# Kernel optimization log

Measured on AMD Instinct MI355X. Metric: run time of the kernel, lower is better.

The kernel has to match this reference:

```python
import jax, jax.numpy as jnp
import numpy as np

B = 256
IN_CH = 1
E = 8          # embedding_channels (power of 2)
DEPTH = 3      # log2(E)
T = 8192       # time_range
WINDOW = 2.0
K = 15         # kernel_size (odd -> torch 'same' == lax 'SAME')
TPI = 2.0 * np.pi


def conv1d(x, w, b, dilation=1, groups=1):
    # x: (B, Cin, T), w: (Cout, Cin/groups, K), b: (Cout,)
    out = jax.lax.conv_general_dilated(
        x, w, window_strides=(1,), padding='SAME',
        rhs_dilation=(dilation,),
        dimension_numbers=('NCH', 'OIH', 'NCH'),
        feature_group_count=groups)
    return out + b[None, :, None]


def setup_inputs() -> dict:
    key = jax.random.key(0)
    ks = jax.random.split(key, 14)
    s = 0.05
    x = jax.random.normal(ks[0], (B, T), jnp.float32)
    W1 = jax.random.normal(ks[1], (E, 2, 1, K), jnp.float32) * s   # per-channel Conv1d(1,2)
    b1 = jax.random.normal(ks[2], (E, 2), jnp.float32) * s
    W2 = jax.random.normal(ks[3], (E, 1, 2, K), jnp.float32) * s   # per-channel Conv1d(2,1)
    b2 = jax.random.normal(ks[4], (E, 1), jnp.float32) * s
    fcW = jax.random.normal(ks[5], (E, 2, T), jnp.float32) * 0.01  # per-channel Linear(T, 2)
    fcb = jax.random.normal(ks[6], (E, 2), jnp.float32) * s
    # deconv tree: level j has 2**(DEPTH-1-j) Conv1d(2,1) units, stacked as grouped conv
    dW0 = jax.random.normal(ks[7], (4, 2, K), jnp.float32) * s
    db0 = jax.random.normal(ks[8], (4,), jnp.float32) * s
    dW1 = jax.random.normal(ks[9], (2, 2, K), jnp.float32) * s
    db1 = jax.random.normal(ks[10], (2,), jnp.float32) * s
    dW2 = jax.random.normal(ks[11], (1, 2, K), jnp.float32) * s
    db2 = jax.random.normal(ks[12], (1,), jnp.float32) * s
    return dict(x=x, W1=W1, b1=b1, W2=W2, b2=b2, fcW=fcW, fcb=fcb,
                dW0=dW0, db0=db0, dW1=dW1, db1=db1, dW2=dW2, db2=db2)


def reference(x, W1, b1, W2, b2, fcW, fcb, dW0, db0, dW1, db1, dW2, db2):
    y = x.reshape(x.shape[0], IN_CH, T)
    # per-channel dilated conv stack (dilation = 2**i)
    chans = []
    for i in range(E):
        h = conv1d(y, W1[i], b1[i], dilation=2 ** i)
        chans.append(conv1d(h, W2[i], b2[i], dilation=2 ** i))
    latent = jnp.concatenate(chans, axis=1)                # (B, E, T)
    # FFT -> frequency / amplitude / offset
    rfft = jnp.fft.rfft(latent, axis=2)                    # (B, E, T//2+1)
    power = jnp.abs(rfft[:, :, 1:]) ** 2
    freqs = jnp.asarray(np.fft.rfftfreq(T)[1:] * T / WINDOW, jnp.float32)
    psum = jnp.sum(power, axis=2)
    f = jnp.sum(freqs * power, axis=2) / psum              # (B, E)
    a = 2.0 * jnp.sqrt(psum) / T
    b_off = rfft.real[:, :, 0] / T
    # per-channel Linear(T, 2) -> phase
    v = jnp.einsum('bet,ect->bec', latent, fcW) + fcb      # (B, E, 2)
    p = jnp.arctan2(v[..., 1], v[..., 0]) / TPI            # (B, E)
    # sinusoid reconstruction
    args = jnp.linspace(-WINDOW / 2, WINDOW / 2, T, dtype=jnp.float32)
    sig = a[..., None] * jnp.sin(TPI * (f[..., None] * args + p[..., None])) + b_off[..., None]
    # deconv tree: pairs of channels -> grouped conv, halving channels each level
    y = sig
    for dW, db in ((dW0, db0), (dW1, db1), (dW2, db2)):
        y = conv1d(y, dW, db, dilation=1, groups=dW.shape[0])
    out = y.reshape(y.shape[0], IN_CH * T)
    return (out, latent, sig,
            p[..., None], f[..., None], a[..., None], b_off[..., None])
```

## Files before the change

kernel.cpp:

```cpp
#include <hip/hip_runtime.h>
#include <math.h>

#define TT 8192
#define BB 256
#define EE 8
#define KK 15
#define PI_F  3.14159265358979323846f
#define TPI_F 6.28318530717958647692f

#define OFF_OUT 0
#define OFF_LAT (BB*TT)
#define OFF_SIG (OFF_LAT + BB*EE*TT)
#define OFF_P   (OFF_SIG + BB*EE*TT)
#define OFF_F   (OFF_P + BB*EE)
#define OFF_A   (OFF_F + BB*EE)
#define OFF_B0  (OFF_A + BB*EE)

#define SWZ(i) ((i) + ((i) >> 5))
#define NF 4096

#define L_RE   0
#define L_IM   4223
#define L_SW   8446
#define L_RBUF 8542
#define L_TOT  8574

__device__ __forceinline__ float rdfl(float v) {
  return __uint_as_float(__builtin_amdgcn_readfirstlane(__float_as_uint(v)));
}

__device__ __forceinline__ int rev4(int k) {
  unsigned r = __brev((unsigned)k) >> 20;
  return (int)(((r & 0x555u) << 1) | ((r >> 1) & 0x555u));
}

__global__ __launch_bounds__(512) void conv_fft_kernel(
    const float* __restrict__ x, const float* __restrict__ W1,
    const float* __restrict__ b1, const float* __restrict__ W2,
    const float* __restrict__ b2, const float* __restrict__ fcW,
    const float* __restrict__ fcb, float* __restrict__ latent,
    float* __restrict__ outP, float* __restrict__ outF,
    float* __restrict__ outA, float* __restrict__ outB0)
{
  extern __shared__ float smem[];
  float* re   = smem + L_RE;
  float* im   = smem + L_IM;
  float* sW   = smem + L_SW;
  float* rbuf = smem + L_RBUF;

  const int e = blockIdx.x, b = blockIdx.y;
  const int d  = 1 << e;
  const int M  = TT >> e;
  const int tid = threadIdx.x;
  const float* xr = x + b * TT;

  if (tid < 29) {
    float acc = 0.0f;
    for (int c = 0; c < 2; c++) {
      const float* w1 = W1 + e*30 + c*15;
      const float* w2 = W2 + e*30 + c*15;
      int jlo = tid - 14; if (jlo < 0) jlo = 0;
      int jhi = tid;      if (jhi > 14) jhi = 14;
      for (int j = jlo; j <= jhi; j++) acc += w2[j] * w1[tid - j];
    }
    sW[tid] = acc;
  } else if (tid == 29) {
    float s20 = 0.f, s21 = 0.f;
    for (int j = 0; j < 15; j++) { s20 += W2[e*30 + j]; s21 += W2[e*30 + 15 + j]; }
    sW[29] = b2[e] + s20*b1[e*2] + s21*b1[e*2 + 1];
  } else if (tid >= 32 && tid < 62) {
    sW[tid] = W1[e*30 + (tid - 32)];
  } else if (tid >= 64 && tid < 94) {
    sW[tid] = W2[e*30 + (tid - 64)];
  } else if (tid == 94 || tid == 95) {
    sW[tid] = b1[e*2 + (tid - 94)];
  }
  __syncthreads();

  float Wc[29];
  #pragma unroll
  for (int s = 0; s < 29; s++) Wc[s] = rdfl(sW[s]);
  const float Bc = rdfl(sW[29]);

  float* lr = latent + (b * EE + e) * TT;

  #pragma unroll 1
  for (int g = 0; g < 4; g++) {
    const int vt = g * 512 + tid;
    const int ph = vt & (d - 1);
    const int m0 = (vt >> e) << 2;
    const float* xp = xr + ph;
    const int nbase = m0 - 14;

    float win[32];
    if (m0 >= 16 && m0 <= M - 20) {
      #pragma unroll
      for (int s = 0; s < 32; s++) win[s] = xp[(nbase + s) * d];
    } else {
      #pragma unroll
      for (int s = 0; s < 32; s++) {
        int ns = nbase + s;
        win[s] = ((unsigned)ns < (unsigned)M) ? xp[ns * d] : 0.0f;
      }
    }

    float acc[4] = {Bc, Bc, Bc, Bc};
    #pragma unroll
    for (int s = 0; s < 29; s++) {
      #pragma unroll
      for (int r = 0; r < 4; r++) acc[r] = fmaf(Wc[s], win[s + r], acc[r]);
    }

    if (m0 <= 6) {
      #pragma unroll
      for (int r = 0; r < 4; r++) {
        float corr = 0.0f;
        #pragma unroll
        for (int j = 0; j < 7; j++) {
          if (m0 + r + j <= 6) {
            float a0 = sW[94], a1 = sW[95];
            #pragma unroll
            for (int k = 0; k < 15; k++) {
              float xv = win[r + j + k];
              a0 = fmaf(sW[32 + k], xv, a0);
              a1 = fmaf(sW[47 + k], xv, a1);
            }
            corr = fmaf(sW[64 + j], a0, corr);
            corr = fmaf(sW[79 + j], a1, corr);
          }
        }
        acc[r] -= corr;
      }
    }
    if (m0 + 3 >= M - 7) {
      #pragma unroll
      for (int r = 0; r < 4; r++) {
        float corr = 0.0f;
        #pragma unroll
        for (int jj = 0; jj < 7; jj++) {
          const int j = 8 + jj;
          if (m0 + r + j >= M + 7) {
            float a0 = sW[94], a1 = sW[95];
            #pragma unroll
            for (int k = 0; k < 15; k++) {
              float xv = win[r + j + k];
              a0 = fmaf(sW[32 + k], xv, a0);
              a1 = fmaf(sW[47 + k], xv, a1);
            }
            corr = fmaf(sW[64 + j], a0, corr);
            corr = fmaf(sW[79 + j], a1, corr);
          }
        }
        acc[r] -= corr;
      }
    }

    #pragma unroll
    for (int r = 0; r < 4; r++) {
      int tg = ph + (m0 + r) * d;
      lr[tg] = acc[r];
      int n  = tg >> 1;
      float* dst = (tg & 1) ? im : re;
      dst[SWZ(n)] = acc[r];
    }
  }
  __syncthreads();

  const float2* f02 = (const float2*)(fcW + (e*2 + 0)*TT);
  const float2* f12 = (const float2*)(fcW + (e*2 + 1)*TT);
  float v0 = 0.f, v1 = 0.f;
  for (int n = tid; n < NF; n += 512) {
    float zr = re[SWZ(n)], zi = im[SWZ(n)];
    float2 a0 = f02[n], a1 = f12[n];
    v0 = fmaf(zr, a0.x, v0); v0 = fmaf(zi, a0.y, v0);
    v1 = fmaf(zr, a1.x, v1); v1 = fmaf(zi, a1.y, v1);
  }
  __syncthreads();

  for (int L = NF >> 2; L >= 1; L >>= 2) {
    float wstep = -1.57079632679f / (float)L;
    for (int u = tid; u < (NF >> 2); u += 512) {
      int p = u & (L - 1);
      int base = ((u - p) << 2) + p;
      int i0 = SWZ(base), i1 = SWZ(base + L), i2 = SWZ(base + 2*L), i3 = SWZ(base + 3*L);
      float ar = re[i0], ai = im[i0];
      float br = re[i1], bi = im[i1];
      float cr = re[i2], ci = im[i2];
      float dr = re[i3], di = im[i3];
      float t0r = ar + cr, t0i = ai + ci;
      float t1r = ar - cr, t1i = ai - ci;
      float t2r = br + dr, t2i = bi + di;
      float t3r = br - dr, t3i = bi - di;
      float A0r = t0r + t2r, A0i = t0i + t2i;
      float A1r = t1r + t3i, A1i = t1i - t3r;
      float A2r = t0r - t2r, A2i = t0i - t2i;
      float A3r = t1r - t3i, A3i = t1i + t3r;
      float ang = wstep * (float)p;
      float s1 = __sinf(ang), c1 = __cosf(ang);
      float c2 = c1*c1 - s1*s1, s2 = 2.f*c1*s1;
      float c3 = c1*c2 - s1*s2, s3 = c1*s2 + s1*c2;
      re[i0] = A0r;                 im[i0] = A0i;
      re[i1] = A1r*c1 - A1i*s1;     im[i1] = A1r*s1 + A1i*c1;
      re[i2] = A2r*c2 - A2i*s2;     im[i2] = A2r*s2 + A2i*c2;
      re[i3] = A3r*c3 - A3i*s3;     im[i3] = A3r*s3 + A3i*c3;
    }
    __syncthreads();
  }

  float pacc = 0.f, facc = 0.f;
  for (int k = 1 + tid; k < NF; k += 512) {
    int jk = SWZ(rev4(k));
    int jm = SWZ(rev4(NF - k));
    float zr = re[jk], zi = im[jk];
    float yr = re[jm], yi = im[jm];
    float Er = 0.5f*(zr + yr), Ei = 0.5f*(zi - yi);
    float Dr = 0.5f*(zr - yr), Di = 0.5f*(zi + yi);
    float Or = Di, Oi = -Dr;
    float ang = -PI_F * (float)k / (float)NF;
    float s = __sinf(ang), c = __cosf(ang);
    float Xr = Er + c*Or - s*Oi;
    float Xi = Ei + c*Oi + s*Or;
    float mag = fmaf(Xr, Xr, Xi*Xi);
    pacc += mag;
    facc = fmaf(0.5f * (float)k, mag, facc);
  }
  if (tid == 0) {
    float X = re[SWZ(0)] - im[SWZ(0)];
    pacc += X*X;
    facc += 2048.0f * X*X;
  }

  #pragma unroll
  for (int off = 32; off > 0; off >>= 1) {
    pacc += __shfl_down(pacc, off);
    facc += __shfl_down(facc, off);
    v0   += __shfl_down(v0, off);
    v1   += __shfl_down(v1, off);
  }
  int wid = tid >> 6, lane = tid & 63;
  if (lane == 0) {
    rbuf[wid*4 + 0] = pacc; rbuf[wid*4 + 1] = facc;
    rbuf[wid*4 + 2] = v0;   rbuf[wid*4 + 3] = v1;
  }
  __syncthreads();
  if (tid == 0) {
    float P = 0.f, Fw = 0.f, V0 = 0.f, V1 = 0.f;
    #pragma unroll
    for (int w = 0; w < 8; w++) {
      P += rbuf[w*4]; Fw += rbuf[w*4+1]; V0 += rbuf[w*4+2]; V1 += rbuf[w*4+3];
    }
    float z0r = re[SWZ(0)], z0i = im[SWZ(0)];
    float amp  = 2.0f * sqrtf(P) / (float)TT;
    float boff = (z0r + z0i) / (float)TT;
    float vv0 = V0 + fcb[e*2 + 0];
    float vv1 = V1 + fcb[e*2 + 1];
    float ph  = atan2f(vv1, vv0) / TPI_F;
    int idx = b*EE + e;
    outP[idx]  = ph;
    outF[idx]  = Fw / P;
    outA[idx]  = amp;
    outB0[idx] = boff;
  }
}

#define TILE_C 512
#define P_S   128
#define P_A   472
#define P_B   616
#define P_TOT 704

__global__ __launch_bounds__(256) void sig_deconv_kernel(
    const float* __restrict__ Pv, const float* __restrict__ Fv,
    const float* __restrict__ Av, const float* __restrict__ B0v,
    const float* __restrict__ dW0, const float* __restrict__ db0,
    const float* __restrict__ dW1, const float* __restrict__ db1,
    const float* __restrict__ dW2, const float* __restrict__ db2,
    float* __restrict__ sig, float* __restrict__ out)
{
  __shared__ float smem[P_TOT];

  const int tile = blockIdx.x, b = blockIdx.y;
  const int t0 = tile * TILE_C;
  const int tid = threadIdx.x;
  const float step = 2.0f / 8191.0f;

  float fs[8], am[8], psh[8], bo[8];
  #pragma unroll
  for (int ch = 0; ch < EE; ch++) {
    int idx = b*EE + ch;
    fs[ch] = Fv[idx]; am[ch] = Av[idx]; psh[ch] = Pv[idx]; bo[ch] = B0v[idx];
  }

  float* hre   = smem;
  float* him   = smem + 24;
  float* ssum  = smem + 48;
  float* Cs    = smem + 72;
  float* Cc    = smem + 80;
  float* chDC  = smem + 88;
  float* bDC   = smem + 96;

  if (tid < 24) {
    int ch  = tid & 7;
    int lvl = tid >> 3;
    const float* w;
    if (lvl == 0)      w = dW0 + (ch >> 1)*30 + (ch & 1)*15;
    else if (lvl == 1) w = dW1 + (ch >> 2)*30 + ((ch >> 1) & 1)*15;
    else               w = dW2 + (ch >> 2)*15;
    float om = TPI_F * fs[ch] * step;
    float ar = 0.f, ai = 0.f, sm = 0.f;
    #pragma unroll
    for (int k = 0; k < 15; k++) {
      float wk = w[k];
      float ang = (float)(k - 7) * om;
      ar = fmaf(wk, __cosf(ang), ar);
      ai = fmaf(wk, __sinf(ang), ai);
      sm += wk;
    }
    hre[tid] = ar; him[tid] = ai; ssum[tid] = sm;
  }
  __syncthreads();

  if (tid < 8) {
    int ch = tid;
    float r0 = hre[ch],      i0 = him[ch];
    float r1 = hre[8 + ch],  i1 = him[8 + ch];
    float r2 = hre[16 + ch], i2 = him[16 + ch];
    float ra = r0*r1 - i0*i1, ia = r0*i1 + i0*r1;
    float rt = ra*r2 - ia*i2, it = ra*i2 + ia*r2;
    Cs[ch] = am[ch] * rt;
    Cc[ch] = am[ch] * it;
    chDC[ch] = bo[ch] * ssum[ch] * ssum[8 + ch] * ssum[16 + ch];
  } else if (tid == 8) {
    float acc = db2[0];
    #pragma unroll
    for (int g0 = 0; g0 < 4; g0++)
      acc = fmaf(db0[g0], ssum[8 + 2*g0] * ssum[16 + 2*g0], acc);
    #pragma unroll
    for (int g1 = 0; g1 < 2; g1++)
      acc = fmaf(db1[g1], ssum[16 + 4*g1], acc);
    bDC[0] = acc;
  }
  __syncthreads();

  float cs[8], cc[8];
  float DC = bDC[0];
  #pragma unroll
  for (int ch = 0; ch < 8; ch++) {
    cs[ch] = Cs[ch]; cc[ch] = Cc[ch]; DC += chDC[ch];
  }

  const int tmin = (tile == 0)  ? 21        : 0;
  const int tmax = (tile == 15) ? (TT - 21) : TT;
  float* orow = out + b*TT;
  #pragma unroll
  for (int it = 0; it < 2; ++it) {
    int t = t0 + it*256 + tid;
    float arg = fmaf(step, (float)t, -1.0f);
    float o = DC;
    #pragma unroll
    for (int ch = 0; ch < 8; ch++) {
      float rr = fmaf(fs[ch], arg, psh[ch]);
      rr -= rintf(rr);
      float th = TPI_F * rr;
      float s = __sinf(th);
      float c = __cosf(th);
      sig[(b*EE + ch)*TT + t] = fmaf(am[ch], s, bo[ch]);
      o = fmaf(s, cs[ch], o);
      o = fmaf(c, cc[ch], o);
    }
    if (t >= tmin && t < tmax) orow[t] = o;
  }

  if (tile == 0) {
    float* Sp = smem + P_S;
    float* Ap = smem + P_A;
    float* Bp = smem + P_B;
    __syncthreads();
    for (int idx = tid; idx < 336; idx += 256) {
      int ch = idx / 42, j = idx - ch*42;
      float arg = fmaf(step, (float)j, -1.0f);
      float rr = fmaf(fs[ch], arg, psh[ch]);
      rr -= rintf(rr);
      Sp[idx] = fmaf(am[ch], __sinf(TPI_F * rr), bo[ch]);
    }
    __syncthreads();
    if (tid < 140) {
      int g = tid / 35, j = tid - g*35;
      float a = db0[g];
      #pragma unroll
      for (int k = 0; k < 15; k++) {
        int is = j + k - 7;
        float s0 = (is >= 0) ? Sp[(2*g)*42 + is]     : 0.0f;
        float s1 = (is >= 0) ? Sp[(2*g+1)*42 + is]   : 0.0f;
        a = fmaf(dW0[g*30 + k],      s0, a);
        a = fmaf(dW0[g*30 + 15 + k], s1, a);
      }
      Ap[tid] = a;
    }
    __syncthreads();
    if (tid < 56) {
      int g1 = tid / 28, j = tid - g1*28;
      float a = db1[g1];
      #pragma unroll
      for (int k = 0; k < 15; k++) {
        int ia = j + k - 7;
        float a0 = (ia >= 0) ? Ap[(2*g1)*35 + ia]   : 0.0f;
        float a1 = (ia >= 0) ? Ap[(2*g1+1)*35 + ia] : 0.0f;
        a = fmaf(dW1[g1*30 + k],      a0, a);
        a = fmaf(dW1[g1*30 + 15 + k], a1, a);
      }
      Bp[tid] = a;
    }
    __syncthreads();
    if (tid < 21) {
      float a = db2[0];
      #pragma unroll
      for (int k = 0; k < 15; k++) {
        int ib = tid + k - 7;
        float b0v_ = (ib >= 0) ? Bp[ib]      : 0.0f;
        float b1v_ = (ib >= 0) ? Bp[28 + ib] : 0.0f;
        a = fmaf(dW2[k],      b0v_, a);
        a = fmaf(dW2[15 + k], b1v_, a);
      }
      orow[tid] = a;
    }
  }
  if (tile == 15) {
    float* Sp = smem + P_S;
    float* Ap = smem + P_A;
    float* Bp = smem + P_B;
    __syncthreads();
    for (int idx = tid; idx < 336; idx += 256) {
      int ch = idx / 42, j = idx - ch*42;
      int t = 8150 + j;
      float arg = fmaf(step, (float)t, -1.0f);
      float rr = fmaf(fs[ch], arg, psh[ch]);
      rr -= rintf(rr);
      Sp[idx] = fmaf(am[ch], __sinf(TPI_F * rr), bo[ch]);
    }
    __syncthreads();
    if (tid < 140) {
      int g = tid / 35, j = tid - g*35;
      float a = db0[g];
      #pragma unroll
      for (int k = 0; k < 15; k++) {
        int is = j + k;
        float s0 = (is < 42) ? Sp[(2*g)*42 + is]   : 0.0f;
        float s1 = (is < 42) ? Sp[(2*g+1)*42 + is] : 0.0f;
        a = fmaf(dW0[g*30 + k],      s0, a);
        a = fmaf(dW0[g*30 + 15 + k], s1, a);
      }
      Ap[tid] = a;
    }
    __syncthreads();
    if (tid < 56) {
      int g1 = tid / 28, j = tid - g1*28;
      float a = db1[g1];
      #pragma unroll
      for (int k = 0; k < 15; k++) {
        int ia = j + k;
        float a0 = (ia < 35) ? Ap[(2*g1)*35 + ia]   : 0.0f;
        float a1 = (ia < 35) ? Ap[(2*g1+1)*35 + ia] : 0.0f;
        a = fmaf(dW1[g1*30 + k],      a0, a);
        a = fmaf(dW1[g1*30 + 15 + k], a1, a);
      }
      Bp[tid] = a;
    }
    __syncthreads();
    if (tid < 21) {
      float a = db2[0];
      #pragma unroll
      for (int k = 0; k < 15; k++) {
        int ib = tid + k;
        float b0v_ = (ib < 28) ? Bp[ib]      : 0.0f;
        float b1v_ = (ib < 28) ? Bp[28 + ib] : 0.0f;
        a = fmaf(dW2[k],      b0v_, a);
        a = fmaf(dW2[15 + k], b1v_, a);
      }
      orow[8171 + tid] = a;
    }
  }
}

extern "C" void kernel_launch(void* const* d_in, const int* in_sizes, int n_in,
                              void* d_out, int out_size, void* d_ws, size_t ws_size,
                              hipStream_t stream) {
  const float* x   = (const float*)d_in[0];
  const float* W1  = (const float*)d_in[1];
  const float* b1  = (const float*)d_in[2];
  const float* W2  = (const float*)d_in[3];
  const float* b2  = (const float*)d_in[4];
  const float* fcW = (const float*)d_in[5];
  const float* fcb = (const float*)d_in[6];
  const float* dW0 = (const float*)d_in[7];
  const float* db0 = (const float*)d_in[8];
  const float* dW1 = (const float*)d_in[9];
  const float* db1 = (const float*)d_in[10];
  const float* dW2 = (const float*)d_in[11];
  const float* db2 = (const float*)d_in[12];

  float* o        = (float*)d_out;
  float* out_main = o + OFF_OUT;
  float* latent   = o + OFF_LAT;
  float* sig      = o + OFF_SIG;
  float* pP  = o + OFF_P;
  float* pF  = o + OFF_F;
  float* pA  = o + OFF_A;
  float* pB0 = o + OFF_B0;

  const size_t lds_fused = L_TOT * sizeof(float);
  conv_fft_kernel<<<dim3(EE, BB), 512, lds_fused, stream>>>(
      x, W1, b1, W2, b2, fcW, fcb, latent, pP, pF, pA, pB0);
  sig_deconv_kernel<<<dim3(TT/TILE_C, BB), 256, 0, stream>>>(
      pP, pF, pA, pB0, dW0, db0, dW1, db1, dW2, db2, sig, out_main);
}
```

Measured before the change: 331.7 us.

## Stage dilated-conv input in LDS by phase for mid dilations, vectorize e=0 loads

For channels with dilation 2, 4 and 8, the input row is copied coalesced into shared memory in two halves, transposed by dilation phase. Each thread then reads its 32-sample window as contiguous float2 loads instead of strided global gathers. For e=0 the window is loaded from global memory with float2 vector loads. This adds about 17 KB of shared memory per block, which may reduce occupancy, plus extra barriers and a duplicated code path.

```diff
diff --git a/kernel.cpp b/kernel.cpp
--- a/kernel.cpp
+++ b/kernel.cpp
@@ -23,7 +23,8 @@
 #define L_IM   4223
 #define L_SW   8446
 #define L_RBUF 8542
-#define L_TOT  8574
+#define L_SXP  8574
+#define L_TOT  12910
 
 __device__ __forceinline__ float rdfl(float v) {
   return __uint_as_float(__builtin_amdgcn_readfirstlane(__float_as_uint(v)));
@@ -47,6 +48,7 @@
   float* im   = smem + L_IM;
   float* sW   = smem + L_SW;
   float* rbuf = smem + L_RBUF;
+  float* sxp  = smem + L_SXP;
 
   const int e = blockIdx.x, b = blockIdx.y;
   const int d  = 1 << e;
@@ -82,89 +84,204 @@
   for (int s = 0; s < 29; s++) Wc[s] = rdfl(sW[s]);
   const float Bc = rdfl(sW[29]);
 
-  float* lr = latent + (b * EE + e) * TT;
-
-  #pragma unroll 1
-  for (int g = 0; g < 4; g++) {
-    const int vt = g * 512 + tid;
-    const int ph = vt & (d - 1);
-    const int m0 = (vt >> e) << 2;
-    const float* xp = xr + ph;
-    const int nbase = m0 - 14;
-
-    float win[32];
-    if (m0 >= 16 && m0 <= M - 20) {
-      #pragma unroll
-      for (int s = 0; s < 32; s++) win[s] = xp[(nbase + s) * d];
-    } else {
-      #pragma unroll
-      for (int s = 0; s < 32; s++) {
-        int ns = nbase + s;
-        win[s] = ((unsigned)ns < (unsigned)M) ? xp[ns * d] : 0.0f;
-      }
-    }
-
-    float acc[4] = {Bc, Bc, Bc, Bc};
-    #pragma unroll
-    for (int s = 0; s < 29; s++) {
-      #pragma unroll
-      for (int r = 0; r < 4; r++) acc[r] = fmaf(Wc[s], win[s + r], acc[r]);
-    }
-
-    if (m0 <= 6) {
+  if (e >= 1 && e <= 3) {
+    const int Mh = (TT/2) >> e;
+    const int Lp = ((((Mh - 2) + 31) >> 5) << 5) + 30;
+
+    #pragma unroll 1
+    for (int h = 0; h < 2; ++h) {
+      const int tbase = h * (TT/2) - 14 * d;
+      const int nstage = (TT/2) + 28 * d;
+      for (int i = tid; i < nstage; i += 512) {
+        int t  = tbase + i;
+        int ph = i & (d - 1);
+        int n  = i >> e;
+        sxp[ph * Lp + n] = (t >= 0 && t < TT) ? xr[t] : 0.0f;
+      }
+      __syncthreads();
+
+      float* lrh = latent + (b * EE + e) * TT + h * (TT/2);
+
+      #pragma unroll 1
+      for (int g = 0; g < 2; g++) {
+        const int vt = g * 512 + tid;
+        const int ph = vt & (d - 1);
+        const int m0 = (vt >> e) << 2;
+
+        float win[32];
+        {
+          const float2* wp = (const float2*)&sxp[ph * Lp + m0];
+          #pragma unroll
+          for (int v = 0; v < 16; v++) {
+            float2 qv = wp[v];
+            win[2*v] = qv.x; win[2*v+1] = qv.y;
+          }
+        }
+        float acc[4] = {Bc, Bc, Bc, Bc};
+        #pragma unroll
+        for (int s = 0; s < 29; s++) {
+          #pragma unroll
+          for (int r = 0; r < 4; r++) acc[r] = fmaf(Wc[s], win[s + r], acc[r]);
+        }
+
+        if (h == 0 && g == 0 && m0 <= 6) {
+          #pragma unroll
+          for (int r = 0; r < 4; r++) {
+            float corr = 0.0f;
+            #pragma unroll
+            for (int j = 0; j < 7; j++) {
+              if (m0 + r + j <= 6) {
+                float a0 = sW[94], a1 = sW[95];
+                #pragma unroll
+                for (int k = 0; k < 15; k++) {
+                  float xv = win[r + j + k];
+                  a0 = fmaf(sW[32 + k], xv, a0);
+                  a1 = fmaf(sW[47 + k], xv, a1);
+                }
+                corr = fmaf(sW[64 + j], a0, corr);
+                corr = fmaf(sW[79 + j], a1, corr);
+              }
+            }
+            acc[r] -= corr;
+          }
+        }
+        if (h == 1 && g == 1 && m0 + 3 >= Mh - 7) {
+          #pragma unroll
+          for (int r = 0; r < 4; r++) {
+            float corr = 0.0f;
+            #pragma unroll
+            for (int jj = 0; jj < 7; jj++) {
+              const int j = 8 + jj;
+              if (m0 + r + j >= Mh + 7) {
+                float a0 = sW[94], a1 = sW[95];
+                #pragma unroll
+                for (int k = 0; k < 15; k++) {
+                  float xv = win[r + j + k];
+                  a0 = fmaf(sW[32 + k], xv, a0);
+                  a1 = fmaf(sW[47 + k], xv, a1);
+                }
+                corr = fmaf(sW[64 + j], a0, corr);
+                corr = fmaf(sW[79 + j], a1, corr);
+              }
+            }
+            acc[r] -= corr;
+          }
+        }
+
+        #pragma unroll
+        for (int r = 0; r < 4; r++) {
+          int toff = ph + (m0 + r) * d;
+          lrh[toff] = acc[r];
+          int tg = h * (TT/2) + toff;
+          int n  = tg >> 1;
+          float* dst = (tg & 1) ? im : re;
+          dst[SWZ(n)] = acc[r];
+        }
+      }
+      __syncthreads();
+    }
+  } else {
+    float* lr = latent + (b * EE + e) * TT;
+
+    #pragma unroll 1
+    for (int g = 0; g < 4; g++) {
+      const int vt = g * 512 + tid;
+      const int ph = vt & (d - 1);
+      const int m0 = (vt >> e) << 2;
+      const int nbase = m0 - 14;
+
+      float win[32];
+      if (e == 0) {
+        if (m0 >= 16 && m0 <= M - 20) {
+          const float2* xq2 = (const float2*)(xr + nbase);
+          #pragma unroll
+          for (int v = 0; v < 16; v++) {
+            float2 qv = xq2[v];
+            win[2*v] = qv.x; win[2*v+1] = qv.y;
+          }
+        } else {
+          #pragma unroll
+          for (int s = 0; s < 32; s++) {
+            int ns = nbase + s;
+            win[s] = ((unsigned)ns < (unsigned)M) ? xr[ns] : 0.0f;
+          }
+        }
+      } else {
+        const float* xp = xr + ph;
+        if (m0 >= 16 && m0 <= M - 20) {
+          #pragma unroll
+          for (int s = 0; s < 32; s++) win[s] = xp[(nbase + s) * d];
+        } else {
+          #pragma unroll
+          for (int s = 0; s < 32; s++) {
+            int ns = nbase + s;
+            win[s] = ((unsigned)ns < (unsigned)M) ? xp[ns * d] : 0.0f;
+          }
+        }
+      }
+
+      float acc[4] = {Bc, Bc, Bc, Bc};
+      #pragma unroll
+      for (int s = 0; s < 29; s++) {
+        #pragma unroll
+        for (int r = 0; r < 4; r++) acc[r] = fmaf(Wc[s], win[s + r], acc[r]);
+      }
+
+      if (m0 <= 6) {
+        #pragma unroll
+        for (int r = 0; r < 4; r++) {
+          float corr = 0.0f;
+          #pragma unroll
+          for (int j = 0; j < 7; j++) {
+            if (m0 + r + j <= 6) {
+              float a0 = sW[94], a1 = sW[95];
+              #pragma unroll
+              for (int k = 0; k < 15; k++) {
+                float xv = win[r + j + k];
+                a0 = fmaf(sW[32 + k], xv, a0);
+                a1 = fmaf(sW[47 + k], xv, a1);
+              }
+              corr = fmaf(sW[64 + j], a0, corr);
+              corr = fmaf(sW[79 + j], a1, corr);
+            }
+          }
+          acc[r] -= corr;
+        }
+      }
+      if (m0 + 3 >= M - 7) {
+        #pragma unroll
+        for (int r = 0; r < 4; r++) {
+          float corr = 0.0f;
+          #pragma unroll
+          for (int jj = 0; jj < 7; jj++) {
+            const int j = 8 + jj;
+            if (m0 + r + j >= M + 7) {
+              float a0 = sW[94], a1 = sW[95];
+              #pragma unroll
+              for (int k = 0; k < 15; k++) {
+                float xv = win[r + j + k];
+                a0 = fmaf(sW[32 + k], xv, a0);
+                a1 = fmaf(sW[47 + k], xv, a1);
+              }
+              corr = fmaf(sW[64 + j], a0, corr);
+              corr = fmaf(sW[79 + j], a1, corr);
+            }
+          }
+          acc[r] -= corr;
+        }
+      }
+
       #pragma unroll
       for (int r = 0; r < 4; r++) {
-        float corr = 0.0f;
-        #pragma unroll
-        for (int j = 0; j < 7; j++) {
-          if (m0 + r + j <= 6) {
-            float a0 = sW[94], a1 = sW[95];
-            #pragma unroll
-            for (int k = 0; k < 15; k++) {
-              float xv = win[r + j + k];
-              a0 = fmaf(sW[32 + k], xv, a0);
-              a1 = fmaf(sW[47 + k], xv, a1);
-            }
-            corr = fmaf(sW[64 + j], a0, corr);
-            corr = fmaf(sW[79 + j], a1, corr);
-          }
-        }
-        acc[r] -= corr;
-      }
-    }
-    if (m0 + 3 >= M - 7) {
-      #pragma unroll
-      for (int r = 0; r < 4; r++) {
-        float corr = 0.0f;
-        #pragma unroll
-        for (int jj = 0; jj < 7; jj++) {
-          const int j = 8 + jj;
-          if (m0 + r + j >= M + 7) {
-            float a0 = sW[94], a1 = sW[95];
-            #pragma unroll
-            for (int k = 0; k < 15; k++) {
-              float xv = win[r + j + k];
-              a0 = fmaf(sW[32 + k], xv, a0);
-              a1 = fmaf(sW[47 + k], xv, a1);
-            }
-            corr = fmaf(sW[64 + j], a0, corr);
-            corr = fmaf(sW[79 + j], a1, corr);
-          }
-        }
-        acc[r] -= corr;
-      }
-    }
-
-    #pragma unroll
-    for (int r = 0; r < 4; r++) {
-      int tg = ph + (m0 + r) * d;
-      lr[tg] = acc[r];
-      int n  = tg >> 1;
-      float* dst = (tg & 1) ? im : re;
-      dst[SWZ(n)] = acc[r];
-    }
-  }
-  __syncthreads();
+        int tg = ph + (m0 + r) * d;
+        lr[tg] = acc[r];
+        int n  = tg >> 1;
+        float* dst = (tg & 1) ? im : re;
+        dst[SWZ(n)] = acc[r];
+      }
+    }
+    __syncthreads();
+  }
 
   const float2* f02 = (const float2*)(fcW + (e*2 + 0)*TT);
   const float2* f12 = (const float2*)(fcW + (e*2 + 1)*TT);
```

Result: faster. 308.1 us (-7.1%).
